# Kernel tuning notes

Measured on AMD Instinct MI355X. Metric: run time of the kernel, lower is better.

Reference implementation:

```python
import jax, jax.numpy as jnp
import numpy as np

B, T, D, HD = 4, 4096, 1024, 64

def setup_inputs() -> dict:
    key = jax.random.key(0)
    kx, kq, kk, kv = jax.random.split(key, 4)
    s = 1.0 / np.sqrt(D)
    return {
        "x": jax.random.normal(kx, (B, T, D), dtype=jnp.float32),
        "wq": jax.random.uniform(kq, (HD, D), jnp.float32, -s, s),
        "wk": jax.random.uniform(kk, (HD, D), jnp.float32, -s, s),
        "wv": jax.random.uniform(kv, (HD, D), jnp.float32, -s, s),
    }

def reference(x, wq, wk, wv):
    # Linear(D, headDim, bias=False): y = x @ W.T with W of shape [headDim, D]
    Q = jnp.einsum('btD,dD->btd', x, wq)
    K = jnp.einsum('bsD,dD->bsd', x, wk)
    V = jnp.einsum('bsD,dD->bsd', x, wv)
    head_dim = wq.shape[0]
    logits = jnp.einsum('btd,bsd->bts', Q, K) / jnp.sqrt(jnp.float32(head_dim))
    attn = jax.nn.softmax(logits, axis=-1)
    return jnp.einsum('bts,bsd->btd', attn, V)
```

## Files before the change

### kernel.cpp

```cpp
#include <hip/hip_runtime.h>
#include <math.h>

#define TLEN 4096
#define BD   1024
#define HDIM 64
#define NB   4

typedef __attribute__((ext_vector_type(8))) short bf16x8;
typedef __attribute__((ext_vector_type(4))) float f32x4;
typedef __attribute__((ext_vector_type(16))) float f32x16;

typedef const __attribute__((address_space(1))) unsigned char* gp_t;
typedef __attribute__((address_space(3))) unsigned char* lp_t;

__device__ __forceinline__ void async_cp16(const void* g, void* l) {
    __builtin_amdgcn_global_load_lds((gp_t)g, (lp_t)l, 16, 0, 0);
}

__device__ __forceinline__ unsigned short f2bf(float f) {
    union { float f; unsigned u; } v; v.f = f;
    unsigned r = v.u + 0x7FFF + ((v.u >> 16) & 1);
    return (unsigned short)(r >> 16);
}

__device__ __forceinline__ bf16x8 cvt8(const float4 a, const float4 b) {
    bf16x8 r;
    r[0] = (short)f2bf(a.x); r[1] = (short)f2bf(a.y);
    r[2] = (short)f2bf(a.z); r[3] = (short)f2bf(a.w);
    r[4] = (short)f2bf(b.x); r[5] = (short)f2bf(b.y);
    r[6] = (short)f2bf(b.z); r[7] = (short)f2bf(b.w);
    return r;
}

__device__ __forceinline__ unsigned cvt_pk_bf16(float lo, float hi) {
    unsigned r;
    asm("v_cvt_pk_bf16_f32 %0, %1, %2" : "=v"(r) : "v"(lo), "v"(hi));
    return r;
}

__global__ __launch_bounds__(256) void wconv_kernel(
    const float* __restrict__ wq, const float* __restrict__ wk,
    const float* __restrict__ wv, unsigned short* __restrict__ wbf)
{
    const int r = blockIdx.x;
    const float* src = (r < 64) ? wq : (r < 128) ? wk : wv;
    const int rr = r & 63;
    const int c  = threadIdx.x * 4;
    float4 a = *(const float4*)&src[(size_t)rr * BD + c];
    uint2 o;
    o.x = (unsigned)f2bf(a.x) | ((unsigned)f2bf(a.y) << 16);
    o.y = (unsigned)f2bf(a.z) | ((unsigned)f2bf(a.w) << 16);
    *(uint2*)&wbf[(size_t)r * BD + c] = o;
}

__global__ __launch_bounds__(256, 2) void qkv_kernel(
    const float* __restrict__ x,
    const unsigned short* __restrict__ wbf,
    unsigned short* __restrict__ Qb,
    unsigned short* __restrict__ Kb,
    unsigned short* __restrict__ Vt)
{
    const int r0   = blockIdx.x * 32;
    const int tid  = threadIdx.x;
    const int lane = tid & 63;
    const int w    = tid >> 6;
    const int g    = lane >> 4;
    const int c    = lane & 15;

    __shared__ __align__(16) unsigned short wsh[2][192 * 64];
    __shared__ __align__(16) float          xf[2][32 * 64];
    __shared__ __align__(16) unsigned short vtr[64][40];

    f32x4 acc[3][2];
    #pragma unroll
    for (int t = 0; t < 3; ++t)
        #pragma unroll
        for (int rg = 0; rg < 2; ++rg) acc[t][rg] = (f32x4){0.f, 0.f, 0.f, 0.f};

    uint4 wreg[6];

    #define LOAD_W(k0s)                                                         \
        {                                                                       \
            _Pragma("unroll")                                                   \
            for (int ii = 0; ii < 6; ++ii) {                                    \
                const int L   = ii * 256 + tid;                                 \
                const int row = L >> 3;                                         \
                const int jl  = (L & 7) ^ (row & 7);                            \
                wreg[ii] = *(const uint4*)&wbf[(size_t)row * BD + (k0s) + jl * 8]; \
            }                                                                   \
        }
    #define WRITE_W(buf)                                                        \
        {                                                                       \
            _Pragma("unroll")                                                   \
            for (int ii = 0; ii < 6; ++ii) {                                    \
                const int L = ii * 256 + tid;                                   \
                *(uint4*)&wsh[buf][L * 8] = wreg[ii];                           \
            }                                                                   \
        }
    #define STAGE_X(buf, k0s)                                                   \
        {                                                                       \
            _Pragma("unroll")                                                   \
            for (int ii = 0; ii < 2; ++ii) {                                    \
                const int L   = ii * 256 + tid;                                 \
                const int row = L >> 4;                                         \
                const int gch = (L & 15) ^ (row & 15);                          \
                async_cp16(&x[(size_t)(r0 + row) * BD + (k0s) + gch * 4],       \
                           &xf[buf][L * 4]);                                    \
            }                                                                   \
        }

    LOAD_W(0)
    STAGE_X(0, 0)
    WRITE_W(0)

    for (int it = 0; it < 16; ++it) {
        const int cb = it & 1;
        __syncthreads();

        if (it < 15) {
            LOAD_W((it + 1) * 64)
            STAGE_X(cb ^ 1, (it + 1) * 64)
        }

        #pragma unroll
        for (int h = 0; h < 2; ++h) {
            const int oct = h * 4 + g;
            bf16x8 aX[2], bW[3];
            #pragma unroll
            for (int rg = 0; rg < 2; ++rg) {
                const int row = rg * 16 + c;
                const float4 a0 = *(const float4*)
                    &xf[cb][row * 64 + ((2 * oct) ^ c) * 4];
                const float4 a1 = *(const float4*)
                    &xf[cb][row * 64 + ((2 * oct + 1) ^ c) * 4];
                aX[rg] = cvt8(a0, a1);
            }
            const int slot = (oct ^ (c & 7)) * 8;
            #pragma unroll
            for (int t = 0; t < 3; ++t)
                bW[t] = *(const bf16x8*)&wsh[cb][((w * 3 + t) * 16 + c) * 64 + slot];
            #pragma unroll
            for (int t = 0; t < 3; ++t)
                #pragma unroll
                for (int rg = 0; rg < 2; ++rg)
                    acc[t][rg] = __builtin_amdgcn_mfma_f32_16x16x32_bf16(
                        aX[rg], bW[t], acc[t][rg], 0, 0, 0);
        }

        if (it < 15) WRITE_W(cb ^ 1)
    }

    const float qscale = 0.18033688f;
    const int   bb     = r0 / TLEN;
    const int   trow   = r0 % TLEN;
    #pragma unroll
    for (int t = 0; t < 3; ++t) {
        const int m = w * 3 + t;
        #pragma unroll
        for (int rg = 0; rg < 2; ++rg)
            #pragma unroll
            for (int i = 0; i < 4; ++i) {
                const int row = rg * 16 + g * 4 + i;
                if (m < 4)
                    Qb[(size_t)(r0 + row) * HDIM + m * 16 + c]
                        = f2bf(acc[t][rg][i] * qscale);
                else if (m < 8)
                    Kb[(size_t)(r0 + row) * HDIM + (m - 4) * 16 + c]
                        = f2bf(acc[t][rg][i]);
                else
                    vtr[(m - 8) * 16 + c][row] = f2bf(acc[t][rg][i]);
            }
    }
    __syncthreads();
    {
        const int d    = tid >> 2;
        const int part = tid & 3;
        uint4 v0 = *(const uint4*)&vtr[d][part * 8];
        unsigned short* dst = Vt + (size_t)bb * HDIM * TLEN + (size_t)d * TLEN
                            + trow + part * 8;
        *(uint4*)&dst[0] = v0;
    }
    #undef LOAD_W
    #undef WRITE_W
    #undef STAGE_X
}

template <int KEYS>
__global__ __launch_bounds__(256, 2) void attn_kernel(
    const unsigned short* __restrict__ Qb,
    const unsigned short* __restrict__ Kb,
    const unsigned short* __restrict__ Vt,
    float* __restrict__ O1, float* __restrict__ Ml, float* __restrict__ out)
{
    const int b     = blockIdx.y;
    const int q0    = blockIdx.x * 128;
    const int split = blockIdx.z;
    const int sbase = split * KEYS;

    const unsigned short* Qp = Qb + (size_t)b * TLEN * HDIM;
    const unsigned short* Kp = Kb + (size_t)b * TLEN * HDIM + (size_t)sbase * HDIM;
    const unsigned short* Vp = Vt + (size_t)b * HDIM * TLEN + sbase;

    const int tid  = threadIdx.x;
    const int lane = tid & 63;
    const int w    = tid >> 6;
    const int ql   = lane & 31;
    const int hi   = lane >> 5;
    const int ch   = lane & 7;

    __shared__ __align__(16) unsigned short ksh[2][4096];
    __shared__ __align__(16) unsigned short vsh[2][4096];

    bf16x8 qB[4];
    #pragma unroll
    for (int s = 0; s < 4; ++s)
        qB[s] = *(const bf16x8*)
            &Qp[(size_t)(q0 + w * 32 + ql) * HDIM + s * 16 + hi * 8];

    float  lsum = 0.f;
    f32x16 oacc[2];
    #pragma unroll
    for (int dt = 0; dt < 2; ++dt)
        #pragma unroll
        for (int i = 0; i < 16; ++i) oacc[dt][i] = 0.f;

    const int nt = KEYS / 64;

    uint4 kreg[2], vreg[2];
    #define LOAD_KV(s0)                                                         \
        {                                                                       \
            _Pragma("unroll")                                                   \
            for (int ii = 0; ii < 2; ++ii) {                                    \
                const int L   = ii * 256 + tid;                                 \
                const int row = L >> 3;                                         \
                const int jl  = (L & 7) ^ (row & 7);                            \
                kreg[ii] = *(const uint4*)&Kp[(size_t)((s0) + row) * HDIM + jl * 8]; \
                vreg[ii] = *(const uint4*)&Vp[(size_t)row * TLEN + (s0) + jl * 8];   \
            }                                                                   \
        }
    #define WRITE_KV(buf)                                                       \
        {                                                                       \
            _Pragma("unroll")                                                   \
            for (int ii = 0; ii < 2; ++ii) {                                    \
                const int L = ii * 256 + tid;                                   \
                *(uint4*)&ksh[buf][L * 8] = kreg[ii];                           \
                *(uint4*)&vsh[buf][L * 8] = vreg[ii];                           \
            }                                                                   \
        }

    LOAD_KV(0)
    WRITE_KV(0)

    for (int it = 0; it < nt; ++it) {
        const int cb = it & 1;
        __syncthreads();

        if (it + 1 < nt) LOAD_KV((it + 1) * 64)

        f32x16 sacc[2];
        #pragma unroll
        for (int kt = 0; kt < 2; ++kt)
            #pragma unroll
            for (int i = 0; i < 16; ++i) sacc[kt][i] = 0.f;
        #pragma unroll
        for (int kt = 0; kt < 2; ++kt)
            #pragma unroll
            for (int s = 0; s < 4; ++s) {
                const bf16x8 kA = *(const bf16x8*)
                    &ksh[cb][(32 * kt + ql) * 64 + ((2 * s + hi) ^ ch) * 8];
                sacc[kt] = __builtin_amdgcn_mfma_f32_32x32x16_bf16(
                    kA, qB[s], sacc[kt], 0, 0, 0);
            }

        if (it + 1 < nt) WRITE_KV(cb ^ 1)

        bf16x8 paf[4];
        #pragma unroll
        for (int kt = 0; kt < 2; ++kt) {
            float p[16];
            #pragma unroll
            for (int i = 0; i < 16; ++i)
                p[i] = __builtin_amdgcn_exp2f(sacc[kt][i]);
            lsum += (((p[0] + p[1]) + (p[2] + p[3]))
                   + ((p[4] + p[5]) + (p[6] + p[7])))
                  + (((p[8] + p[9]) + (p[10] + p[11]))
                   + ((p[12] + p[13]) + (p[14] + p[15])));
            #pragma unroll
            for (int bb = 0; bb < 2; ++bb) {
                const unsigned X0 = cvt_pk_bf16(p[8 * bb + 0], p[8 * bb + 1]);
                const unsigned X1 = cvt_pk_bf16(p[8 * bb + 2], p[8 * bb + 3]);
                const unsigned Z0 = cvt_pk_bf16(p[8 * bb + 4], p[8 * bb + 5]);
                const unsigned Z1 = cvt_pk_bf16(p[8 * bb + 6], p[8 * bb + 7]);
                auto s02 = __builtin_amdgcn_permlane32_swap(X0, Z0, false, false);
                auto s13 = __builtin_amdgcn_permlane32_swap(X1, Z1, false, false);
                union { unsigned u[4]; bf16x8 v; } pu;
                pu.u[0] = s02[0]; pu.u[1] = s13[0];
                pu.u[2] = s02[1]; pu.u[3] = s13[1];
                paf[kt * 2 + bb] = pu.v;
            }
        }

        #pragma unroll
        for (int dt = 0; dt < 2; ++dt)
            #pragma unroll
            for (int s = 0; s < 4; ++s) {
                const bf16x8 vB = *(const bf16x8*)
                    &vsh[cb][(32 * dt + ql) * 64 + ((2 * s + hi) ^ ch) * 8];
                oacc[dt] = __builtin_amdgcn_mfma_f32_32x32x16_bf16(
                    paf[s], vB, oacc[dt], 0, 0, 0);
            }
    }
    #undef LOAD_KV
    #undef WRITE_KV

    lsum += __shfl_xor(lsum, 32);

    if (KEYS == TLEN) {
        #pragma unroll
        for (int r = 0; r < 16; ++r) {
            const int   qr   = (r & 3) + 8 * (r >> 2) + 4 * hi;
            const float inv  = 1.0f / __shfl(lsum, qr);
            const size_t orow = (size_t)b * TLEN + q0 + w * 32 + qr;
            out[orow * HDIM + ql]      = oacc[0][r] * inv;
            out[orow * HDIM + 32 + ql] = oacc[1][r] * inv;
        }
    } else {
        float* Od = (split == 0)
            ? out : O1 + (size_t)(split - 1) * NB * TLEN * HDIM;
        #pragma unroll
        for (int r = 0; r < 16; ++r) {
            const int   qr   = (r & 3) + 8 * (r >> 2) + 4 * hi;
            const size_t orow = (size_t)b * TLEN + q0 + w * 32 + qr;
            Od[orow * HDIM + ql]      = oacc[0][r];
            Od[orow * HDIM + 32 + ql] = oacc[1][r];
        }
        if (lane < 32)
            Ml[(size_t)(split * NB + b) * TLEN + q0 + w * 32 + lane] = lsum;
    }
}

__global__ __launch_bounds__(256) void merge_kernel(
    float* __restrict__ out, const float* __restrict__ O1,
    const float* __restrict__ Ml)
{
    const int idx  = blockIdx.x * 256 + threadIdx.x;
    const int row  = idx >> 4;
    const int col4 = (idx & 15) * 4;
    const int b    = row >> 12;
    const int t    = row & (TLEN - 1);
    float l = 0.f;
    #pragma unroll
    for (int s = 0; s < 4; ++s) l += Ml[(size_t)(s * NB + b) * TLEN + t];
    const float inv = 1.0f / l;
    float4 a = *(const float4*)&out[(size_t)row * HDIM + col4];
    #pragma unroll
    for (int s = 1; s < 4; ++s) {
        float4 p = *(const float4*)
            &O1[(size_t)(s - 1) * NB * TLEN * HDIM + (size_t)row * HDIM + col4];
        a.x += p.x; a.y += p.y; a.z += p.z; a.w += p.w;
    }
    a.x *= inv; a.y *= inv; a.z *= inv; a.w *= inv;
    *(float4*)&out[(size_t)row * HDIM + col4] = a;
}

extern "C" void kernel_launch(void* const* d_in, const int* in_sizes, int n_in,
                              void* d_out, int out_size, void* d_ws, size_t ws_size,
                              hipStream_t stream)
{
    (void)in_sizes; (void)n_in; (void)out_size;
    const float* x  = (const float*)d_in[0];
    const float* wq = (const float*)d_in[1];
    const float* wk = (const float*)d_in[2];
    const float* wv = (const float*)d_in[3];
    float* out = (float*)d_out;

    unsigned short* wbf = (unsigned short*)d_out;
    unsigned short* Qbf = (unsigned short*)d_ws;
    unsigned short* Kbf = Qbf + (size_t)NB * TLEN * HDIM;
    unsigned short* Vtb = Kbf + (size_t)NB * TLEN * HDIM;
    float* Ml = (float*)((char*)d_ws + (size_t)3 * NB * TLEN * HDIM * 2);
    float* O1 = Ml + (size_t)4 * NB * TLEN;
    const size_t ws_need = (size_t)3 * NB * TLEN * HDIM * 2
                         + (size_t)4 * NB * TLEN * 4
                         + (size_t)3 * NB * TLEN * HDIM * 4;
    const bool use_split = ws_size >= ws_need;

    wconv_kernel<<<dim3(192), 256, 0, stream>>>(wq, wk, wv, wbf);
    qkv_kernel<<<dim3(NB * TLEN / 32), 256, 0, stream>>>(x, wbf, Qbf, Kbf, Vtb);

    if (use_split) {
        attn_kernel<TLEN / 4><<<dim3(TLEN / 128, NB, 4), 256, 0, stream>>>(
            Qbf, Kbf, Vtb, O1, Ml, out);
        merge_kernel<<<dim3(NB * TLEN * 16 / 256), 256, 0, stream>>>(out, O1, Ml);
    } else {
        attn_kernel<TLEN><<<dim3(TLEN / 128, NB, 1), 256, 0, stream>>>(
            Qbf, Kbf, Vtb, O1, Ml, out);
    }
}
```

Baseline: 144.7 us.

## Load QKV weights straight to registers, use packed bf16 converts, add MFMA priority hints

The QKV projection kernel stops staging the bf16 weight tile through shared memory. Each wave now loads its own weight fragments from global memory into double-buffered registers, and the loop is manually unrolled by two to alternate between the buffers. The fp32-to-bf16 conversions now use the packed v_cvt_pk_bf16_f32 instruction instead of bit-manipulation rounding. The attention kernel wraps its MFMA sections in s_setprio hints. The changes aim to cut LDS traffic, extra syncs and ALU conversion cost, at the price of more registers and redundant global weight reads across waves.

After: 151.9 us. 1.05x slower.

```diff
diff --git a/kernel.cpp b/kernel.cpp
--- a/kernel.cpp
+++ b/kernel.cpp
@@ -23,19 +23,19 @@
     return (unsigned short)(r >> 16);
 }
 
-__device__ __forceinline__ bf16x8 cvt8(const float4 a, const float4 b) {
-    bf16x8 r;
-    r[0] = (short)f2bf(a.x); r[1] = (short)f2bf(a.y);
-    r[2] = (short)f2bf(a.z); r[3] = (short)f2bf(a.w);
-    r[4] = (short)f2bf(b.x); r[5] = (short)f2bf(b.y);
-    r[6] = (short)f2bf(b.z); r[7] = (short)f2bf(b.w);
-    return r;
-}
-
 __device__ __forceinline__ unsigned cvt_pk_bf16(float lo, float hi) {
     unsigned r;
     asm("v_cvt_pk_bf16_f32 %0, %1, %2" : "=v"(r) : "v"(lo), "v"(hi));
     return r;
+}
+
+__device__ __forceinline__ bf16x8 cvt8pk(const float4 a, const float4 b) {
+    union { unsigned u[4]; bf16x8 v; } r;
+    r.u[0] = cvt_pk_bf16(a.x, a.y);
+    r.u[1] = cvt_pk_bf16(a.z, a.w);
+    r.u[2] = cvt_pk_bf16(b.x, b.y);
+    r.u[3] = cvt_pk_bf16(b.z, b.w);
+    return r.v;
 }
 
 __global__ __launch_bounds__(256) void wconv_kernel(
@@ -48,8 +48,8 @@
     const int c  = threadIdx.x * 4;
     float4 a = *(const float4*)&src[(size_t)rr * BD + c];
     uint2 o;
-    o.x = (unsigned)f2bf(a.x) | ((unsigned)f2bf(a.y) << 16);
-    o.y = (unsigned)f2bf(a.z) | ((unsigned)f2bf(a.w) << 16);
+    o.x = cvt_pk_bf16(a.x, a.y);
+    o.y = cvt_pk_bf16(a.z, a.w);
     *(uint2*)&wbf[(size_t)r * BD + c] = o;
 }
 
@@ -67,35 +67,29 @@
     const int g    = lane >> 4;
     const int c    = lane & 15;
 
-    __shared__ __align__(16) unsigned short wsh[2][192 * 64];
     __shared__ __align__(16) float          xf[2][32 * 64];
     __shared__ __align__(16) unsigned short vtr[64][40];
 
+    int wrow[3];
+    #pragma unroll
+    for (int t = 0; t < 3; ++t) wrow[t] = (w * 3 + t) * 16 + c;
+
     f32x4 acc[3][2];
     #pragma unroll
     for (int t = 0; t < 3; ++t)
         #pragma unroll
         for (int rg = 0; rg < 2; ++rg) acc[t][rg] = (f32x4){0.f, 0.f, 0.f, 0.f};
 
-    uint4 wreg[6];
-
-    #define LOAD_W(k0s)                                                         \
-        {                                                                       \
-            _Pragma("unroll")                                                   \
-            for (int ii = 0; ii < 6; ++ii) {                                    \
-                const int L   = ii * 256 + tid;                                 \
-                const int row = L >> 3;                                         \
-                const int jl  = (L & 7) ^ (row & 7);                            \
-                wreg[ii] = *(const uint4*)&wbf[(size_t)row * BD + (k0s) + jl * 8]; \
-            }                                                                   \
-        }
-    #define WRITE_W(buf)                                                        \
-        {                                                                       \
-            _Pragma("unroll")                                                   \
-            for (int ii = 0; ii < 6; ++ii) {                                    \
-                const int L = ii * 256 + tid;                                   \
-                *(uint4*)&wsh[buf][L * 8] = wreg[ii];                           \
-            }                                                                   \
+    uint4 wfA[6], wfB[6];
+
+    #define LOAD_WF(W, k0s)                                                     \
+        {                                                                       \
+            _Pragma("unroll")                                                   \
+            for (int t = 0; t < 3; ++t)                                         \
+                _Pragma("unroll")                                               \
+                for (int h = 0; h < 2; ++h)                                     \
+                    W[t * 2 + h] = *(const uint4*)                              \
+                        &wbf[(size_t)wrow[t] * BD + (k0s) + (h * 4 + g) * 8];   \
         }
     #define STAGE_X(buf, k0s)                                                   \
         {                                                                       \
@@ -109,45 +103,44 @@
             }                                                                   \
         }
 
-    LOAD_W(0)
+    #define QKV_BODY(itv, cbv, WCUR, WNXT)                                      \
+        {                                                                       \
+            __syncthreads();                          \
+            if ((itv) < 15) {                                                   \
+                STAGE_X((cbv) ^ 1, ((itv) + 1) * 64)                            \
+                LOAD_WF(WNXT, ((itv) + 1) * 64)                                 \
+            }                                                                   \
+            _Pragma("unroll")                                                   \
+            for (int h = 0; h < 2; ++h) {                                       \
+                const int oct = h * 4 + g;                                      \
+                bf16x8 aX[2];                                                   \
+                _Pragma("unroll")                                               \
+                for (int rg = 0; rg < 2; ++rg) {                                \
+                    const int row = rg * 16 + c;                                \
+                    const float4 a0 = *(const float4*)                          \
+                        &xf[cbv][row * 64 + ((2 * oct) ^ c) * 4];               \
+                    const float4 a1 = *(const float4*)                          \
+                        &xf[cbv][row * 64 + ((2 * oct + 1) ^ c) * 4];           \
+                    aX[rg] = cvt8pk(a0, a1);                                    \
+                }                                                               \
+                _Pragma("unroll")                                               \
+                for (int t = 0; t < 3; ++t) {                                   \
+                    const bf16x8 bW = *(const bf16x8*)&WCUR[t * 2 + h];         \
+                    _Pragma("unroll")                                           \
+                    for (int rg = 0; rg < 2; ++rg)                              \
+                        acc[t][rg] = __builtin_amdgcn_mfma_f32_16x16x32_bf16(   \
+                            aX[rg], bW, acc[t][rg], 0, 0, 0);                   \
+                }                                                               \
+            }                                                                   \
+        }
+
+    LOAD_WF(wfA, 0)
     STAGE_X(0, 0)
-    WRITE_W(0)
-
-    for (int it = 0; it < 16; ++it) {
-        const int cb = it & 1;
-        __syncthreads();
-
-        if (it < 15) {
-            LOAD_W((it + 1) * 64)
-            STAGE_X(cb ^ 1, (it + 1) * 64)
-        }
-
-        #pragma unroll
-        for (int h = 0; h < 2; ++h) {
-            const int oct = h * 4 + g;
-            bf16x8 aX[2], bW[3];
-            #pragma unroll
-            for (int rg = 0; rg < 2; ++rg) {
-                const int row = rg * 16 + c;
-                const float4 a0 = *(const float4*)
-                    &xf[cb][row * 64 + ((2 * oct) ^ c) * 4];
-                const float4 a1 = *(const float4*)
-                    &xf[cb][row * 64 + ((2 * oct + 1) ^ c) * 4];
-                aX[rg] = cvt8(a0, a1);
-            }
-            const int slot = (oct ^ (c & 7)) * 8;
-            #pragma unroll
-            for (int t = 0; t < 3; ++t)
-                bW[t] = *(const bf16x8*)&wsh[cb][((w * 3 + t) * 16 + c) * 64 + slot];
-            #pragma unroll
-            for (int t = 0; t < 3; ++t)
-                #pragma unroll
-                for (int rg = 0; rg < 2; ++rg)
-                    acc[t][rg] = __builtin_amdgcn_mfma_f32_16x16x32_bf16(
-                        aX[rg], bW[t], acc[t][rg], 0, 0, 0);
-        }
-
-        if (it < 15) WRITE_W(cb ^ 1)
+
+    #pragma unroll
+    for (int it2 = 0; it2 < 8; ++it2) {
+        QKV_BODY(2 * it2,     0, wfA, wfB)
+        QKV_BODY(2 * it2 + 1, 1, wfB, wfA)
     }
 
     const float qscale = 0.18033688f;
@@ -180,9 +173,9 @@
                             + trow + part * 8;
         *(uint4*)&dst[0] = v0;
     }
-    #undef LOAD_W
-    #undef WRITE_W
+    #undef LOAD_WF
     #undef STAGE_X
+    #undef QKV_BODY
 }
 
 template <int KEYS>
@@ -262,6 +255,7 @@
         for (int kt = 0; kt < 2; ++kt)
             #pragma unroll
             for (int i = 0; i < 16; ++i) sacc[kt][i] = 0.f;
+        __builtin_amdgcn_s_setprio(1);
         #pragma unroll
         for (int kt = 0; kt < 2; ++kt)
             #pragma unroll
@@ -271,6 +265,7 @@
                 sacc[kt] = __builtin_amdgcn_mfma_f32_32x32x16_bf16(
                     kA, qB[s], sacc[kt], 0, 0, 0);
             }
+        __builtin_amdgcn_s_setprio(0);
 
         if (it + 1 < nt) WRITE_KV(cb ^ 1)
 
@@ -300,6 +295,7 @@
             }
         }
 
+        __builtin_amdgcn_s_setprio(1);
         #pragma unroll
         for (int dt = 0; dt < 2; ++dt)
             #pragma unroll
@@ -309,6 +305,7 @@
                 oacc[dt] = __builtin_amdgcn_mfma_f32_32x32x16_bf16(
                     paf[s], vB, oacc[dt], 0, 0, 0);
             }
+        __builtin_amdgcn_s_setprio(0);
     }
     #undef LOAD_KV
     #undef WRITE_KV
```

## Use packed bf16 converts, register-staged x loads, and MFMA wave priority

Applied to the files above, without the earlier changes.

Three separate changes. Scalar float-to-bf16 rounding is replaced by the packed v_cvt_pk_bf16_f32 instruction in the weight conversion and in the QKV projection's A-operand conversion, which cuts VALU work. The x tile is now prefetched through registers and written to LDS after the MFMAs, instead of going through global_load_lds async copies. In the attention kernel, s_setprio raises wave priority around the MFMA blocks so matrix work gets scheduled ahead of other waves. The register staging adds VGPR pressure and an extra LDS write, and rounding behaviour may differ slightly from the hand-written f2bf.

After: 140.4 us. 1.03x faster.

```diff
diff --git a/kernel.cpp b/kernel.cpp
--- a/kernel.cpp
+++ b/kernel.cpp
@@ -10,32 +10,25 @@
 typedef __attribute__((ext_vector_type(4))) float f32x4;
 typedef __attribute__((ext_vector_type(16))) float f32x16;
 
-typedef const __attribute__((address_space(1))) unsigned char* gp_t;
-typedef __attribute__((address_space(3))) unsigned char* lp_t;
-
-__device__ __forceinline__ void async_cp16(const void* g, void* l) {
-    __builtin_amdgcn_global_load_lds((gp_t)g, (lp_t)l, 16, 0, 0);
-}
-
 __device__ __forceinline__ unsigned short f2bf(float f) {
     union { float f; unsigned u; } v; v.f = f;
     unsigned r = v.u + 0x7FFF + ((v.u >> 16) & 1);
     return (unsigned short)(r >> 16);
 }
 
-__device__ __forceinline__ bf16x8 cvt8(const float4 a, const float4 b) {
-    bf16x8 r;
-    r[0] = (short)f2bf(a.x); r[1] = (short)f2bf(a.y);
-    r[2] = (short)f2bf(a.z); r[3] = (short)f2bf(a.w);
-    r[4] = (short)f2bf(b.x); r[5] = (short)f2bf(b.y);
-    r[6] = (short)f2bf(b.z); r[7] = (short)f2bf(b.w);
-    return r;
-}
-
 __device__ __forceinline__ unsigned cvt_pk_bf16(float lo, float hi) {
     unsigned r;
     asm("v_cvt_pk_bf16_f32 %0, %1, %2" : "=v"(r) : "v"(lo), "v"(hi));
     return r;
+}
+
+__device__ __forceinline__ bf16x8 cvt8pk(const float4 a, const float4 b) {
+    union { unsigned u[4]; bf16x8 v; } r;
+    r.u[0] = cvt_pk_bf16(a.x, a.y);
+    r.u[1] = cvt_pk_bf16(a.z, a.w);
+    r.u[2] = cvt_pk_bf16(b.x, b.y);
+    r.u[3] = cvt_pk_bf16(b.z, b.w);
+    return r.v;
 }
 
 __global__ __launch_bounds__(256) void wconv_kernel(
@@ -48,8 +41,8 @@
     const int c  = threadIdx.x * 4;
     float4 a = *(const float4*)&src[(size_t)rr * BD + c];
     uint2 o;
-    o.x = (unsigned)f2bf(a.x) | ((unsigned)f2bf(a.y) << 16);
-    o.y = (unsigned)f2bf(a.z) | ((unsigned)f2bf(a.w) << 16);
+    o.x = cvt_pk_bf16(a.x, a.y);
+    o.y = cvt_pk_bf16(a.z, a.w);
     *(uint2*)&wbf[(size_t)r * BD + c] = o;
 }
 
@@ -77,7 +70,7 @@
         #pragma unroll
         for (int rg = 0; rg < 2; ++rg) acc[t][rg] = (f32x4){0.f, 0.f, 0.f, 0.f};
 
-    uint4 wreg[6];
+    uint4 wreg[6], xreg[2];
 
     #define LOAD_W(k0s)                                                         \
         {                                                                       \
@@ -97,21 +90,29 @@
                 *(uint4*)&wsh[buf][L * 8] = wreg[ii];                           \
             }                                                                   \
         }
-    #define STAGE_X(buf, k0s)                                                   \
+    #define LOAD_X(k0s)                                                         \
         {                                                                       \
             _Pragma("unroll")                                                   \
             for (int ii = 0; ii < 2; ++ii) {                                    \
                 const int L   = ii * 256 + tid;                                 \
                 const int row = L >> 4;                                         \
                 const int gch = (L & 15) ^ (row & 15);                          \
-                async_cp16(&x[(size_t)(r0 + row) * BD + (k0s) + gch * 4],       \
-                           &xf[buf][L * 4]);                                    \
+                xreg[ii] = *(const uint4*)&x[(size_t)(r0 + row) * BD + (k0s) + gch * 4]; \
+            }                                                                   \
+        }
+    #define WRITE_X(buf)                                                        \
+        {                                                                       \
+            _Pragma("unroll")                                                   \
+            for (int ii = 0; ii < 2; ++ii) {                                    \
+                const int L = ii * 256 + tid;                                   \
+                *(uint4*)&xf[buf][L * 4] = xreg[ii];                            \
             }                                                                   \
         }
 
     LOAD_W(0)
-    STAGE_X(0, 0)
+    LOAD_X(0)
     WRITE_W(0)
+    WRITE_X(0)
 
     for (int it = 0; it < 16; ++it) {
         const int cb = it & 1;
@@ -119,7 +120,7 @@
 
         if (it < 15) {
             LOAD_W((it + 1) * 64)
-            STAGE_X(cb ^ 1, (it + 1) * 64)
+            LOAD_X((it + 1) * 64)
         }
 
         #pragma unroll
@@ -133,7 +134,7 @@
                     &xf[cb][row * 64 + ((2 * oct) ^ c) * 4];
                 const float4 a1 = *(const float4*)
                     &xf[cb][row * 64 + ((2 * oct + 1) ^ c) * 4];
-                aX[rg] = cvt8(a0, a1);
+                aX[rg] = cvt8pk(a0, a1);
             }
             const int slot = (oct ^ (c & 7)) * 8;
             #pragma unroll
@@ -147,7 +148,10 @@
                         aX[rg], bW[t], acc[t][rg], 0, 0, 0);
         }
 
-        if (it < 15) WRITE_W(cb ^ 1)
+        if (it < 15) {
+            WRITE_W(cb ^ 1)
+            WRITE_X(cb ^ 1)
+        }
     }
 
     const float qscale = 0.18033688f;
@@ -182,7 +186,8 @@
     }
     #undef LOAD_W
     #undef WRITE_W
-    #undef STAGE_X
+    #undef LOAD_X
+    #undef WRITE_X
 }
 
 template <int KEYS>
@@ -262,6 +267,7 @@
         for (int kt = 0; kt < 2; ++kt)
             #pragma unroll
             for (int i = 0; i < 16; ++i) sacc[kt][i] = 0.f;
+        __builtin_amdgcn_s_setprio(1);
         #pragma unroll
         for (int kt = 0; kt < 2; ++kt)
             #pragma unroll
@@ -271,6 +277,7 @@
                 sacc[kt] = __builtin_amdgcn_mfma_f32_32x32x16_bf16(
                     kA, qB[s], sacc[kt], 0, 0, 0);
             }
+        __builtin_amdgcn_s_setprio(0);
 
         if (it + 1 < nt) WRITE_KV(cb ^ 1)
 
@@ -300,6 +307,7 @@
             }
         }
 
+        __builtin_amdgcn_s_setprio(1);
         #pragma unroll
         for (int dt = 0; dt < 2; ++dt)
             #pragma unroll
@@ -309,6 +317,7 @@
                 oacc[dt] = __builtin_amdgcn_mfma_f32_32x32x16_bf16(
                     paf[s], vB, oacc[dt], 0, 0, 0);
             }
+        __builtin_amdgcn_s_setprio(0);
     }
     #undef LOAD_KV
     #undef WRITE_KV
```
